# Optimization experiments

Measured on AMD Instinct MI355X. Metric: run time of the kernel, lower is better.

The kernel has to match this reference:

```python
import jax, jax.numpy as jnp
import numpy as np

N = 200_000   # total nodes across batched AIGs
E = 400_000   # edges (fan-in ~2 per gate)
D = 64        # input_dim == dim_hidden (required by in-place scatter in _gru_forward)
B = 16        # number of graphs in batch
LF = 12       # num forward topological levels
LB = 12       # num backward topological levels
NUM_ROUNDS = 1


def setup_inputs() -> dict:
    key = jax.random.key(0)
    ks = jax.random.split(key, 9)
    node_type = jax.random.randint(ks[0], (N,), 0, 3, dtype=jnp.int32)
    num_inverted_predecessors = jax.random.randint(ks[1], (N,), 0, 3, dtype=jnp.int32)
    edge_index = jax.random.randint(ks[2], (2, E), 0, N, dtype=jnp.int32)
    forward_level = jax.random.randint(ks[3], (N,), 0, LF, dtype=jnp.int32)
    backward_level = jax.random.randint(ks[4], (N,), 0, LB, dtype=jnp.int32)
    batch = jnp.sort(jax.random.randint(ks[5], (N,), 0, B, dtype=jnp.int32))
    s = 1.0 / np.sqrt(D)
    W_enc = jax.random.normal(ks[6], (2, D), dtype=jnp.float32) * 0.5
    b_enc = jnp.zeros((D,), dtype=jnp.float32)
    W_f = jax.random.normal(ks[7], (D, D), dtype=jnp.float32) * s
    b_f = jnp.zeros((D,), dtype=jnp.float32)
    W_b = jax.random.normal(ks[8], (D, D), dtype=jnp.float32) * s
    b_b = jnp.zeros((D,), dtype=jnp.float32)
    return dict(node_type=node_type,
                num_inverted_predecessors=num_inverted_predecessors,
                edge_index=edge_index,
                forward_level=forward_level,
                backward_level=backward_level,
                batch=batch,
                W_enc=W_enc, b_enc=b_enc,
                W_f=W_f, b_f=b_f,
                W_b=W_b, b_b=b_b)


def reference(node_type, num_inverted_predecessors, edge_index,
              forward_level, backward_level, batch,
              W_enc, b_enc, W_f, b_f, W_b, b_b):
    # h_init = node_encoder(cat(node_type, num_inverted_predecessors))
    x = jnp.stack([node_type, num_inverted_predecessors], axis=1).astype(W_enc.dtype)  # [N,2]
    h = x @ W_enc + b_enc  # [N,D] node_state
    src, dst = edge_index[0], edge_index[1]

    for _ in range(NUM_ROUNDS):
        # forward topological sweep: level l nodes receive sum of mlp(h_src)
        # over incoming edges whose destination is at level l (subgraph dim=1).
        for l in range(1, LF):
            m = h @ W_f + b_f                                    # AggConv mlp on current state
            e_w = (forward_level[dst] == l).astype(h.dtype)      # edges into level-l nodes
            msg = jax.ops.segment_sum(m[src] * e_w[:, None], dst, num_segments=N)
            h = jnp.where((forward_level == l)[:, None], msg, h)  # scatter l_msg into node_state
        # backward sweep (reverse flow): level-l sources receive sum of
        # mlp_b(h_dst) over outgoing edges (subgraph dim=0, target_to_source).
        for l in range(1, LB):
            m = h @ W_b + b_b
            e_w = (backward_level[src] == l).astype(h.dtype)
            msg = jax.ops.segment_sum(m[dst] * e_w[:, None], src, num_segments=N)
            h = jnp.where((backward_level == l)[:, None], msg, h)

    # readout over output nodes (node_type == 1): [global_max_pool, global_add_pool]
    out_mask = (node_type == 1)
    neg_inf = jnp.finfo(h.dtype).min
    max_pool = jax.ops.segment_max(jnp.where(out_mask[:, None], h, neg_inf), batch, num_segments=B)
    sum_pool = jax.ops.segment_sum(h * out_mask[:, None].astype(h.dtype), batch, num_segments=B)
    return jnp.concatenate([max_pool, sum_pool], axis=1)  # [B, 2*D]
```

## Files before the change

### kernel.cpp

```cpp
#include <hip/hip_runtime.h>
#include <float.h>

#define NLVL 12
#define NB   16
#define NBLK 256
#define EBLK 2048
#define FG   1024


struct Params {
    const int *nt, *ninv, *src, *dst, *fl, *bl, *batch;
    const float *We, *be, *Wf, *bf, *Wb, *bb;
    float *hN, *hB, *tabg, *out;
    int *rowptr, *cursor, *col, *nb_f, *nb_b, *onodes, *bsums, *bsums2, *meta, *plarr, *bar;
    int *deg, *rowscan;
    int *cntf, *cntb, *cnto, *blkf, *blkb, *blko;
    int *blkFf, *blkFb, *blkFo;
    int N, E, M, outN;
};

__device__ __forceinline__ float rlanef(float x, int l) {
    return __int_as_float(__builtin_amdgcn_readlane(__float_as_int(x), l));
}
__device__ __forceinline__ void sti(int* a, int v) {
    __hip_atomic_store(a, v, __ATOMIC_RELAXED, __HIP_MEMORY_SCOPE_AGENT);
}
__device__ __forceinline__ void stf(float* a, float v) {
    __hip_atomic_store(a, v, __ATOMIC_RELAXED, __HIP_MEMORY_SCOPE_AGENT);
}
__device__ __forceinline__ int ald(int* a) {
    return __hip_atomic_load(a, __ATOMIC_RELAXED, __HIP_MEMORY_SCOPE_AGENT);
}
__device__ __forceinline__ int afa(int* a, int v) {
    return __hip_atomic_fetch_add(a, v, __ATOMIC_RELAXED, __HIP_MEMORY_SCOPE_AGENT);
}

__device__ __forceinline__ void gbar3(int* bar, int nblk, int t) {
    __syncthreads();
    if (threadIdx.x == 0) {
        const int line = blockIdx.x & 15;
        const int per  = nblk >> 4;
        int a = afa(&bar[line * 32], 1);
        if (a == per * t - 1) {
            int m = afa(&bar[16 * 32], 1);
            if (m == 16 * t - 1) {
                sti(&bar[17 * 32], t);
            } else {
                while (ald(&bar[17 * 32]) < t) __builtin_amdgcn_s_sleep(1);
            }
            for (int b = line; b < nblk; b += 16)
                sti(&bar[(18 + b) * 32], t);
        } else {
            while (ald(&bar[(18 + blockIdx.x) * 32]) < t) __builtin_amdgcn_s_sleep(4);
        }
    }
    asm volatile("" ::: "memory");
    __syncthreads();
}

__device__ __forceinline__ int blockScanIncl(int v, int* s, int t) {
    s[t] = v; __syncthreads();
    for (int off = 1; off < 256; off <<= 1) {
        int add = (t >= off) ? s[t - off] : 0; __syncthreads();
        s[t] += add; __syncthreads();
    }
    int r = s[t]; __syncthreads();
    return r;
}

template <int DIR>
__device__ __forceinline__ void sweep_level(const Params& p, int lvl,
                                            const float (&w)[64], float bv,
                                            int lane, int wid, int nw, int q, int fb) {
    const int* nb = DIR ? p.nb_b : p.nb_f;
    const int* rp = p.rowptr + (DIR ? p.N : 0);
    int start = p.meta[(DIR ? 128 : 96) + lvl];
    int cnt   = p.meta[(DIR ? 128 : 96) + lvl + 1] - start;
    float* db = DIR ? p.hB : p.hN;
    const int e2 = 2 * p.E;

    int c0 = (int)((long long)cnt * wid / nw);
    int c1 = (int)((long long)cnt * (wid + 1) / nw);
    for (int i = c0; i < c1; i += 4) {
        int my = i + q;
        int v = 0, rpv = 0, rpe = 0;
        if (my < c1) {
            int e = nb[start + my];
            v = e & 0x3FFFF;
            rpv = rp[v]; rpe = rp[v + 1];
            rpv = (rpv < 0) ? 0 : (rpv > e2 ? e2 : rpv);
            rpe = (rpe < rpv) ? rpv : (rpe > e2 ? e2 : rpe);
            if (rpe > rpv + 4096) rpe = rpv + 4096;
        }
        float4 acc = make_float4(0.f, 0.f, 0.f, 0.f);
        for (int cb = rpv; cb < rpe; cb++) {
            int cu = p.col[cb];
            int u = cu & 0x3FFFF;
            int flu = (cu >> 18) & 15, blu = (cu >> 22) & 15;
            const float* sp;
            if (DIR == 0)
                sp = (flu > 0 && flu < lvl) ? (p.hN + (size_t)u * 64)
                                            : (p.tabg + ((cu >> 26) & 15) * 64);
            else
                sp = (blu > 0 && blu < lvl) ? (p.hB + (size_t)u * 64)
                   : (flu > 0)              ? (p.hN + (size_t)u * 64)
                                            : (p.tabg + ((cu >> 26) & 15) * 64);
            const float4 x = *(const float4*)(sp + fb);
            acc.x += x.x; acc.y += x.y; acc.z += x.z; acc.w += x.w;
        }
        #pragma unroll
        for (int qq = 0; qq < 4; qq++) {
            if (i + qq >= c1) break;
            int vs   = __builtin_amdgcn_readlane(v, 16 * qq);
            int degs = __builtin_amdgcn_readlane(rpe, 16 * qq)
                     - __builtin_amdgcn_readlane(rpv, 16 * qq);
            float o = bv * (float)degs;
            #pragma unroll
            for (int m = 0; m < 16; m++) {
                float ax = rlanef(acc.x, 16 * qq + m);
                float ay = rlanef(acc.y, 16 * qq + m);
                float az = rlanef(acc.z, 16 * qq + m);
                float aw = rlanef(acc.w, 16 * qq + m);
                o = fmaf(ax, w[4 * m + 0], o);
                o = fmaf(ay, w[4 * m + 1], o);
                o = fmaf(az, w[4 * m + 2], o);
                o = fmaf(aw, w[4 * m + 3], o);
            }
            stf(&db[(size_t)vs * 64 + lane], o);
        }
    }
}

__device__ inline void atomicMaxF(float* addr, float val) {
    int* ai = (int*)addr;
    int old = *ai;
    while (__int_as_float(old) < val) {
        int assumed = old;
        old = atomicCAS(ai, assumed, __float_as_int(val));
        if (old == assumed) break;
    }
}

__device__ __forceinline__ void readout_body(const Params& p, int bid, int tid) {
    int lane = tid & 63;
    int b = bid >> 5;
    int sl = bid & 31;
    int a0 = p.meta[160 + b], a1 = p.meta[161 + b];
    a0 = (a0 < 0) ? 0 : (a0 > p.N ? p.N : a0);
    a1 = (a1 < a0) ? a0 : (a1 > p.N ? p.N : a1);
    int cnt = a1 - a0;
    if (cnt == 0) return;
    int lo = a0 + (int)((long long)cnt * sl / 32);
    int hi = a0 + (int)((long long)cnt * (sl + 1) / 32);
    int wcnt = hi - lo;
    int wave = tid >> 6;
    int wl = lo + (wcnt * wave) / 4;
    int wh = lo + (wcnt * (wave + 1)) / 4;
    if (wh <= wl) return;
    float mx = -FLT_MAX, sm = 0.f;
    for (int k = wl; k < wh; k += 64) {
        int take = wh - k; if (take > 64) take = 64;
        int el = (lane < take) ? p.onodes[k + lane] : 0;
        for (int j = 0; j < take; j++) {
            int e = __shfl(el, j, 64);
            int v = e & 0x3FFFF;
            int flv = (e >> 18) & 15, blv = (e >> 22) & 15;
            const float* sp = (blv > 0) ? (p.hB + (size_t)v * 64)
                            : (flv > 0) ? (p.hN + (size_t)v * 64)
                                        : (p.tabg + ((e >> 26) & 15) * 64);
            float x = sp[lane];
            mx = fmaxf(mx, x);
            sm += x;
        }
    }
    atomicMaxF(&p.out[b * 128 + lane], mx);
    atomicAdd(&p.out[b * 128 + 64 + lane], sm);
}

__global__ __launch_bounds__(256) __attribute__((amdgpu_waves_per_eu(4, 4)))
void k_fused(Params p) {
    const int tid = threadIdx.x, bid = blockIdx.x;
    const int lane = tid & 63;
    int* bar = p.bar;
    int ep = 0;
    __shared__ int s[256];
    __shared__ int hist[40];
    __shared__ int cur[48];

    if (tid < 40) hist[tid] = 0;
    __syncthreads();
    for (int e = bid * 256 + tid; e < p.E; e += FG * 256) {
        atomicAdd(&p.deg[p.dst[e]], 1);
        atomicAdd(&p.deg[p.N + p.src[e]], 1);
    }
    for (int i = bid * 256 + tid; i < p.outN; i += FG * 256)
        stf(&p.out[i], ((i & 127) < 64) ? -FLT_MAX : 0.0f);
    if (bid == 0 && tid < 64) {
        #pragma unroll
        for (int row = 0; row < 9; row++) {
            float nf = (float)(row / 3), iv = (float)(row % 3);
            stf(&p.tabg[row * 64 + tid],
                fmaf(nf, p.We[tid], fmaf(iv, p.We[64 + tid], p.be[tid])));
        }
    }
    if (bid < NBLK) {
        int chunk = (p.N + NBLK - 1) / NBLK;
        int lo = bid * chunk, hi = lo + chunk; if (hi > p.N) hi = p.N;
        for (int i = lo + tid; i < hi; i += 256) {
            int f = p.fl[i], b = p.bl[i];
            int t2 = p.nt[i], iv = p.ninv[i];
            sti(&p.plarr[i], f | (b << 4) | ((t2 * 3 + iv) << 8));
            atomicAdd(&hist[f], 1);
            atomicAdd(&hist[12 + b], 1);
            if (t2 == 1) atomicAdd(&hist[24 + p.batch[i]], 1);
        }
    }
    __syncthreads();
    if (bid < NBLK) {
        if (tid < NLVL) { sti(&p.cntf[tid * NBLK + bid], hist[tid]); sti(&p.cntb[tid * NBLK + bid], hist[12 + tid]); }
        if (tid < NB) sti(&p.cnto[tid * NBLK + bid], hist[24 + tid]);
    }
    gbar3(bar, FG, ++ep);

    const int nscan = (p.M + 511) >> 9;
    if (bid < nscan) {
        int g0 = (bid << 9) + tid * 2;
        int e0 = (g0 < p.M) ? p.deg[g0] : 0;
        int e1 = (g0 + 1 < p.M) ? p.deg[g0 + 1] : 0;
        int incl = blockScanIncl(e0 + e1, s, tid);
        int excl = incl - (e0 + e1);
        if (g0 < p.M) sti(&p.rowscan[g0], excl);
        if (g0 + 1 < p.M) sti(&p.rowscan[g0 + 1], excl + e0);
        if (tid == 255) sti(&p.bsums[bid], incl);
    } else if (bid >= nscan + 2 && bid < nscan + 2 + 2 * NLVL + NB) {
        int j = bid - (nscan + 2);
        const int* sA; int* dA;
        if (j < NLVL)          { sA = p.cntf + j * NBLK;              dA = p.blkf + j * NBLK; }
        else if (j < 2 * NLVL) { sA = p.cntb + (j - NLVL) * NBLK;     dA = p.blkb + (j - NLVL) * NBLK; }
        else                   { sA = p.cnto + (j - 2 * NLVL) * NBLK; dA = p.blko + (j - 2 * NLVL) * NBLK; }
        int v = sA[tid];
        int incl = blockScanIncl(v, s, tid);
        sti(&dA[tid], incl - v);
        if (tid == 255) sti(&p.meta[224 + j], incl);
    }
    gbar3(bar, FG, ++ep);

    if (bid == 0) {
        int i0 = tid * 4;
        int a0 = (i0     < nscan) ? p.bsums[i0]     : 0;
        int a1 = (i0 + 1 < nscan) ? p.bsums[i0 + 1] : 0;
        int a2 = (i0 + 2 < nscan) ? p.bsums[i0 + 2] : 0;
        int a3 = (i0 + 3 < nscan) ? p.bsums[i0 + 3] : 0;
        int incl = blockScanIncl(a0 + a1 + a2 + a3, s, tid);
        int b0 = incl - (a0 + a1 + a2 + a3);
        if (i0     < nscan) sti(&p.bsums2[i0],     b0);
        if (i0 + 1 < nscan) sti(&p.bsums2[i0 + 1], b0 + a0);
        if (i0 + 2 < nscan) sti(&p.bsums2[i0 + 2], b0 + a0 + a1);
        if (i0 + 3 < nscan) sti(&p.bsums2[i0 + 3], b0 + a0 + a1 + a2);
    } else if (bid == 1 && tid < 3) {
        if (tid == 0) { int a = 0; for (int l = 0; l < NLVL; l++) { sti(&p.meta[96 + l], a);  a += p.meta[224 + l]; }            sti(&p.meta[96 + NLVL], a); }
        if (tid == 1) { int a = 0; for (int l = 0; l < NLVL; l++) { sti(&p.meta[128 + l], a); a += p.meta[224 + NLVL + l]; }     sti(&p.meta[128 + NLVL], a); }
        if (tid == 2) { int a = 0; for (int l = 0; l < NB; l++)   { sti(&p.meta[160 + l], a); a += p.meta[224 + 2 * NLVL + l]; } sti(&p.meta[160 + NB], a); }
    }
    gbar3(bar, FG, ++ep);

    for (int g = bid * 256 + tid; g < p.M; g += FG * 256) {
        int r = p.rowscan[g] + p.bsums2[g >> 9];
        sti(&p.rowptr[g], r);
        sti(&p.cursor[g], r);
    }
    if (bid == 0 && tid == 0) sti(&p.rowptr[p.M], 2 * p.E);
    for (int i = bid * 256 + tid; i < NLVL * NBLK; i += FG * 256) {
        sti(&p.blkFf[i], p.blkf[i] + p.meta[96 + (i >> 8)]);
        sti(&p.blkFb[i], p.blkb[i] + p.meta[128 + (i >> 8)]);
    }
    for (int i = bid * 256 + tid; i < NB * NBLK; i += FG * 256)
        sti(&p.blkFo[i], p.blko[i] + p.meta[160 + (i >> 8)]);
    gbar3(bar, FG, ++ep);

    for (int e = bid * 256 + tid; e < p.E; e += FG * 256) {
        int sN = p.src[e], d = p.dst[e];
        sti(&p.col[atomicAdd(&p.cursor[d], 1)],         sN | (p.plarr[sN] << 18));
        sti(&p.col[atomicAdd(&p.cursor[p.N + sN], 1)],   d | (p.plarr[d]  << 18));
    }
    if (bid < NBLK) {
        if (tid < NLVL) { cur[tid] = p.blkFf[tid * NBLK + bid]; cur[16 + tid] = p.blkFb[tid * NBLK + bid]; }
        if (tid < NB) cur[32 + tid] = p.blkFo[tid * NBLK + bid];
        __syncthreads();
        int chunk = (p.N + NBLK - 1) / NBLK;
        int lo = bid * chunk, hi = lo + chunk; if (hi > p.N) hi = p.N;
        for (int i = lo + tid; i < hi; i += 256) {
            int pl = p.plarr[i];
            int lf = pl & 15, lb = (pl >> 4) & 15, tx = (pl >> 8) & 15;
            int pk = i | (pl << 18);
            sti(&p.nb_f[atomicAdd(&cur[lf], 1)], pk);
            sti(&p.nb_b[atomicAdd(&cur[16 + lb], 1)], pk);
            if (tx >= 3 && tx < 6)
                sti(&p.onodes[atomicAdd(&cur[32 + p.batch[i]], 1)], pk);
        }
    }
    gbar3(bar, FG, ++ep);

    const int wid = (bid * 256 + tid) >> 6;
    const int nw  = (FG * 256) >> 6;
    const int q = lane >> 4, fb = (lane & 15) * 4;
    {
        float w[64];
        #pragma unroll
        for (int k = 0; k < 64; k++) w[k] = p.Wf[k * 64 + lane];
        float bv = p.bf[lane];
        for (int lvl = 1; lvl < NLVL; lvl++) {
            sweep_level<0>(p, lvl, w, bv, lane, wid, nw, q, fb);
            gbar3(bar, FG, ++ep);
        }
    }
    {
        float w[64];
        #pragma unroll
        for (int k = 0; k < 64; k++) w[k] = p.Wb[k * 64 + lane];
        float bv = p.bb[lane];
        for (int lvl = 1; lvl < NLVL; lvl++) {
            sweep_level<1>(p, lvl, w, bv, lane, wid, nw, q, fb);
            gbar3(bar, FG, ++ep);
        }
    }

    if (bid < NB * 32) readout_body(p, bid, tid);
}

__global__ void k_edge_deg(Params p) {
    int g = blockIdx.x * 256 + threadIdx.x, gs = gridDim.x * 256;
    for (int e = g; e < p.E; e += gs) {
        atomicAdd(&p.rowptr[p.dst[e]], 1);
        atomicAdd(&p.rowptr[p.N + p.src[e]], 1);
    }
}

__global__ void k_deg_hist(Params p) {
    __shared__ int hf[NLVL], hb[NLVL], ho[NB];
    int tid = threadIdx.x, bid = blockIdx.x;
    if (tid < NLVL) { hf[tid] = 0; hb[tid] = 0; }
    if (tid < NB) ho[tid] = 0;
    __syncthreads();
    int chunk = (p.N + gridDim.x - 1) / gridDim.x;
    int lo = bid * chunk, hi = lo + chunk; if (hi > p.N) hi = p.N;
    for (int i = lo + tid; i < hi; i += 256) {
        int f = p.fl[i], b = p.bl[i];
        int t = p.nt[i], iv = p.ninv[i];
        p.plarr[i] = f | (b << 4) | ((t * 3 + iv) << 8);
        atomicAdd(&hf[f], 1);
        atomicAdd(&hb[b], 1);
        if (t == 1) atomicAdd(&ho[p.batch[i]], 1);
    }
    __syncthreads();
    if (tid < NLVL) { p.cntf[tid * NBLK + bid] = hf[tid]; p.cntb[tid * NBLK + bid] = hb[tid]; }
    if (tid < NB) p.cnto[tid * NBLK + bid] = ho[tid];
}

__global__ void k_scan1(int* __restrict__ data, int M, int* __restrict__ bsums) {
    __shared__ int s[512];
    int t = threadIdx.x;
    int g = blockIdx.x * 512 + t;
    int v = (g < M) ? data[g] : 0;
    s[t] = v;
    __syncthreads();
    for (int off = 1; off < 512; off <<= 1) {
        int add = (t >= off) ? s[t - off] : 0;
        __syncthreads();
        s[t] += add;
        __syncthreads();
    }
    if (g < M) data[g] = s[t] - v;
    if (t == 511) bsums[blockIdx.x] = s[511];
}

__global__ void k_scan_top(int* __restrict__ bsums, int nblk, Params p,
                           float* __restrict__ out, int outN) {
    __shared__ int s[1024];
    __shared__ int tot[48];
    int t = threadIdx.x;
    int* meta = p.meta;
    for (int i = t; i < outN; i += 1024)
        out[i] = ((i & 127) < 64) ? -FLT_MAX : 0.0f;
    if (t < 576) {
        int row = t >> 6, j = t & 63;
        float nf = (float)(row / 3), iv = (float)(row % 3);
        p.tabg[t] = fmaf(nf, p.We[j], fmaf(iv, p.We[64 + j], p.be[j]));
    }
    int seg = t >> 8, b = t & 255;
    for (int r = 0; r < 3; r++) {
        int l = 4 * r + seg;
        int v = p.cntf[l * NBLK + b];
        s[t] = v; __syncthreads();
        for (int off = 1; off < NBLK; off <<= 1) {
            int add = (b >= off) ? s[t - off] : 0; __syncthreads();
            s[t] += add; __syncthreads();
        }
        p.blkf[l * NBLK + b] = s[t] - v;
        if (b == NBLK - 1) tot[l] = s[t];
        __syncthreads();
    }
    for (int r = 0; r < 3; r++) {
        int l = 4 * r + seg;
        int v = p.cntb[l * NBLK + b];
        s[t] = v; __syncthreads();
        for (int off = 1; off < NBLK; off <<= 1) {
            int add = (b >= off) ? s[t - off] : 0; __syncthreads();
            s[t] += add; __syncthreads();
        }
        p.blkb[l * NBLK + b] = s[t] - v;
        if (b == NBLK - 1) tot[16 + l] = s[t];
        __syncthreads();
    }
    for (int r = 0; r < 4; r++) {
        int l = 4 * r + seg;
        int v = p.cnto[l * NBLK + b];
        s[t] = v; __syncthreads();
        for (int off = 1; off < NBLK; off <<= 1) {
            int add = (b >= off) ? s[t - off] : 0; __syncthreads();
            s[t] += add; __syncthreads();
        }
        p.blko[l * NBLK + b] = s[t] - v;
        if (b == NBLK - 1) tot[32 + l] = s[t];
        __syncthreads();
    }
    if (t == 0) { int a = 0; for (int l = 0; l < NLVL; l++) { meta[96 + l] = a; a += tot[l]; } meta[96 + NLVL] = a; }
    if (t == 1) { int a = 0; for (int l = 0; l < NLVL; l++) { meta[128 + l] = a; a += tot[16 + l]; } meta[128 + NLVL] = a; }
    if (t == 2) { int a = 0; for (int l = 0; l < NB; l++) { meta[160 + l] = a; a += tot[32 + l]; } meta[160 + NB] = a; }
    __syncthreads();
    for (int i = t; i < NLVL * NBLK; i += 1024) p.blkf[i] += meta[96 + (i >> 8)];
    for (int i = t; i < NLVL * NBLK; i += 1024) p.blkb[i] += meta[128 + (i >> 8)];
    for (int i = t; i < NB * NBLK; i += 1024) p.blko[i] += meta[160 + (i >> 8)];
    int v = (t < nblk) ? bsums[t] : 0;
    s[t] = v;
    __syncthreads();
    for (int off = 1; off < 1024; off <<= 1) {
        int add = (t >= off) ? s[t - off] : 0;
        __syncthreads();
        s[t] += add;
        __syncthreads();
    }
    if (t < nblk) bsums[t] = s[t] - v;
}

__global__ void k_scan_add(int* __restrict__ rowptr, int* __restrict__ cursor, int M, int total,
                           const int* __restrict__ bsums) {
    int g = blockIdx.x * blockDim.x + threadIdx.x;
    if (g >= M) return;
    int r = rowptr[g] + bsums[g >> 9];
    rowptr[g] = r;
    cursor[g] = r;
    if (g == 0) rowptr[M] = total;
}

__global__ void k_edge_fill(Params p) {
    int g = blockIdx.x * 256 + threadIdx.x, gs = gridDim.x * 256;
    int N = p.N;
    for (int e = g; e < p.E; e += gs) {
        int s = p.src[e], d = p.dst[e];
        p.col[atomicAdd(&p.cursor[d], 1)] = s | (p.plarr[s] << 18);
        p.col[atomicAdd(&p.cursor[N + s], 1)] = d | (p.plarr[d] << 18);
    }
}

__global__ void k_fill(Params p) {
    __shared__ int cur[48];
    int tid = threadIdx.x, bid = blockIdx.x;
    int N = p.N;
    if (tid < NLVL) { cur[tid] = p.blkf[tid * NBLK + bid]; cur[16 + tid] = p.blkb[tid * NBLK + bid]; }
    if (tid < NB) cur[32 + tid] = p.blko[tid * NBLK + bid];
    __syncthreads();
    int chunk = (N + gridDim.x - 1) / gridDim.x;
    int lo = bid * chunk, hi = lo + chunk; if (hi > N) hi = N;
    for (int i = lo + tid; i < hi; i += 256) {
        int pl = p.plarr[i];
        int lf = pl & 15, lb = (pl >> 4) & 15, tx = (pl >> 8) & 15;
        int pk = i | (pl << 18);
        p.nb_f[atomicAdd(&cur[lf], 1)] = pk;
        p.nb_b[atomicAdd(&cur[16 + lb], 1)] = pk;
        if (tx >= 3 && tx < 6)
            p.onodes[atomicAdd(&cur[32 + p.batch[i]], 1)] = pk;
    }
}

__global__ __launch_bounds__(256) __attribute__((amdgpu_waves_per_eu(4, 4)))
void k_sweep(Params p, int lvl, int dir) {
    const int tid = threadIdx.x, lane = tid & 63;
    const float* W = dir ? p.Wb : p.Wf;
    float w[64];
    #pragma unroll
    for (int k = 0; k < 64; k++) w[k] = W[k * 64 + lane];
    float bv = (dir ? p.bb : p.bf)[lane];
    const int wid = (blockIdx.x * 256 + tid) >> 6;
    const int nw  = (gridDim.x * 256) >> 6;
    const int q = lane >> 4, fb = (lane & 15) * 4;
    if (dir == 0) sweep_level<0>(p, lvl, w, bv, lane, wid, nw, q, fb);
    else          sweep_level<1>(p, lvl, w, bv, lane, wid, nw, q, fb);
}

__global__ void k_readout(Params p) {
    readout_body(p, blockIdx.x, threadIdx.x);
}

extern "C" void kernel_launch(void* const* d_in, const int* in_sizes, int n_in,
                              void* d_out, int out_size, void* d_ws, size_t ws_size,
                              hipStream_t stream) {
    int N = in_sizes[0];
    int E = in_sizes[2] / 2;
    int M = 2 * N;

    Params p;
    p.nt    = (const int*)d_in[0];
    p.ninv  = (const int*)d_in[1];
    p.src   = (const int*)d_in[2];
    p.dst   = (const int*)d_in[2] + E;
    p.fl    = (const int*)d_in[3];
    p.bl    = (const int*)d_in[4];
    p.batch = (const int*)d_in[5];
    p.We    = (const float*)d_in[6];
    p.be    = (const float*)d_in[7];
    p.Wf    = (const float*)d_in[8];
    p.bf    = (const float*)d_in[9];
    p.Wb    = (const float*)d_in[10];
    p.bb    = (const float*)d_in[11];
    p.out   = (float*)d_out;
    p.N = N; p.E = E; p.M = M; p.outN = out_size;

    char* ws = (char*)d_ws;
    size_t off = 0;
    auto alloc = [&](size_t bytes) -> char* {
        char* q = ws + off;
        off = (off + bytes + 255) & ~(size_t)255;
        return q;
    };
    p.rowptr = (int*)  alloc((size_t)(M + 1) * sizeof(int));
    p.deg    = (int*)  alloc((size_t)M * sizeof(int));
    p.meta   = (int*)  alloc(512 * sizeof(int));
    p.bar    = (int*)  alloc((size_t)(18 + FG) * 32 * sizeof(int));
    size_t zbytes = (size_t)((char*)(p.bar + (18 + FG) * 32) - (char*)p.rowptr);
    p.hN     = (float*)alloc((size_t)N * 64 * sizeof(float));
    p.hB     = (float*)alloc((size_t)N * 64 * sizeof(float));
    p.tabg   = (float*)alloc(9 * 64 * sizeof(float));
    p.cursor = (int*)  alloc((size_t)M * sizeof(int));
    p.rowscan= (int*)  alloc((size_t)M * sizeof(int));
    p.col    = (int*)  alloc((size_t)2 * E * sizeof(int));
    p.nb_f   = (int*)  alloc((size_t)N * sizeof(int));
    p.nb_b   = (int*)  alloc((size_t)N * sizeof(int));
    p.onodes = (int*)  alloc((size_t)N * sizeof(int));
    p.plarr  = (int*)  alloc((size_t)N * sizeof(int));
    p.bsums  = (int*)  alloc(1024 * sizeof(int));
    p.bsums2 = (int*)  alloc(1024 * sizeof(int));
    p.cntf   = (int*)  alloc(NLVL * NBLK * sizeof(int));
    p.cntb   = (int*)  alloc(NLVL * NBLK * sizeof(int));
    p.cnto   = (int*)  alloc(NB * NBLK * sizeof(int));
    p.blkf   = (int*)  alloc(NLVL * NBLK * sizeof(int));
    p.blkb   = (int*)  alloc(NLVL * NBLK * sizeof(int));
    p.blko   = (int*)  alloc(NB * NBLK * sizeof(int));
    p.blkFf  = (int*)  alloc(NLVL * NBLK * sizeof(int));
    p.blkFb  = (int*)  alloc(NLVL * NBLK * sizeof(int));
    p.blkFo  = (int*)  alloc(NB * NBLK * sizeof(int));

    int nscan = (M + 511) / 512;

    static int g_fused = -2;
    if (g_fused == -2) {
        int mb = 0;
        g_fused = 0;
        if (hipOccupancyMaxActiveBlocksPerMultiprocessor(&mb, k_fused, 256, 0) == hipSuccess
                && mb > 0) {
            int dev = 0;
            hipGetDevice(&dev);
            hipDeviceProp_t props;
            if (hipGetDeviceProperties(&props, dev) == hipSuccess &&
                (long)mb * props.multiProcessorCount >= FG)
                g_fused = 1;
        }
    }

    hipMemsetAsync(p.rowptr, 0, zbytes, stream);
    if (g_fused == 1) {
        k_fused<<<FG, 256, 0, stream>>>(p);
    } else {
        k_edge_deg<<<EBLK, 256, 0, stream>>>(p);
        k_deg_hist<<<NBLK, 256, 0, stream>>>(p);
        k_scan1<<<nscan, 512, 0, stream>>>(p.rowptr, M, p.bsums);
        k_scan_top<<<1, 1024, 0, stream>>>(p.bsums, nscan, p, p.out, out_size);
        k_scan_add<<<(M + 255) / 256, 256, 0, stream>>>(p.rowptr, p.cursor, M, 2 * E, p.bsums);
        k_edge_fill<<<EBLK, 256, 0, stream>>>(p);
        k_fill<<<NBLK, 256, 0, stream>>>(p);
        for (int l = 1; l < NLVL; l++)
            k_sweep<<<1024, 256, 0, stream>>>(p, l, 0);
        for (int l = 1; l < NLVL; l++)
            k_sweep<<<1024, 256, 0, stream>>>(p, l, 1);
        k_readout<<<NB * 32, 256, 0, stream>>>(p);
    }
}
```

Baseline: 496.7 us.

## Spread node bucketing over all fused blocks and widen grid barrier fan-in

Node histogramming and level/batch bucketing now run on all 1024 blocks instead of only 256, so per-block count and offset arrays grow to FG entries and the offset scan handles four values per thread. The separate pass that materialised final block offsets (blkF*) and the arrays behind it are removed; each block adds the level base from meta when it loads its cursors. The grid barrier uses 32 arrival counters instead of 16, which reduces contention on each counter. The aim is shorter serial phases during CSR and bucket construction, at the cost of more, smaller histogram writes and more work in the offset scan.

```diff
diff --git a/kernel.cpp b/kernel.cpp
--- a/kernel.cpp
+++ b/kernel.cpp
@@ -6,6 +6,7 @@
 #define NBLK 256
 #define EBLK 2048
 #define FG   1024
+#define BARLINES 32
 
 
 struct Params {
@@ -15,7 +16,6 @@
     int *rowptr, *cursor, *col, *nb_f, *nb_b, *onodes, *bsums, *bsums2, *meta, *plarr, *bar;
     int *deg, *rowscan;
     int *cntf, *cntb, *cnto, *blkf, *blkb, *blko;
-    int *blkFf, *blkFb, *blkFo;
     int N, E, M, outN;
 };
 
@@ -35,23 +35,23 @@
     return __hip_atomic_fetch_add(a, v, __ATOMIC_RELAXED, __HIP_MEMORY_SCOPE_AGENT);
 }
 
-__device__ __forceinline__ void gbar3(int* bar, int nblk, int t) {
+__device__ __forceinline__ void gbar3(int* bar, int t) {
     __syncthreads();
     if (threadIdx.x == 0) {
-        const int line = blockIdx.x & 15;
-        const int per  = nblk >> 4;
+        const int line = blockIdx.x & (BARLINES - 1);
+        const int per  = FG / BARLINES;
         int a = afa(&bar[line * 32], 1);
         if (a == per * t - 1) {
-            int m = afa(&bar[16 * 32], 1);
-            if (m == 16 * t - 1) {
-                sti(&bar[17 * 32], t);
+            int m = afa(&bar[BARLINES * 32], 1);
+            if (m == BARLINES * t - 1) {
+                sti(&bar[(BARLINES + 1) * 32], t);
             } else {
-                while (ald(&bar[17 * 32]) < t) __builtin_amdgcn_s_sleep(1);
+                while (ald(&bar[(BARLINES + 1) * 32]) < t) __builtin_amdgcn_s_sleep(1);
             }
-            for (int b = line; b < nblk; b += 16)
-                sti(&bar[(18 + b) * 32], t);
+            for (int b = line; b < FG; b += BARLINES)
+                sti(&bar[(BARLINES + 2 + b) * 32], t);
         } else {
-            while (ald(&bar[(18 + blockIdx.x) * 32]) < t) __builtin_amdgcn_s_sleep(4);
+            while (ald(&bar[(BARLINES + 2 + blockIdx.x) * 32]) < t) __builtin_amdgcn_s_sleep(4);
         }
     }
     asm volatile("" ::: "memory");
@@ -203,8 +203,8 @@
                 fmaf(nf, p.We[tid], fmaf(iv, p.We[64 + tid], p.be[tid])));
         }
     }
-    if (bid < NBLK) {
-        int chunk = (p.N + NBLK - 1) / NBLK;
+    {
+        const int chunk = (p.N + FG - 1) / FG;
         int lo = bid * chunk, hi = lo + chunk; if (hi > p.N) hi = p.N;
         for (int i = lo + tid; i < hi; i += 256) {
             int f = p.fl[i], b = p.bl[i];
@@ -216,11 +216,9 @@
         }
     }
     __syncthreads();
-    if (bid < NBLK) {
-        if (tid < NLVL) { sti(&p.cntf[tid * NBLK + bid], hist[tid]); sti(&p.cntb[tid * NBLK + bid], hist[12 + tid]); }
-        if (tid < NB) sti(&p.cnto[tid * NBLK + bid], hist[24 + tid]);
-    }
-    gbar3(bar, FG, ++ep);
+    if (tid < NLVL) { sti(&p.cntf[tid * FG + bid], hist[tid]); sti(&p.cntb[tid * FG + bid], hist[12 + tid]); }
+    if (tid < NB) sti(&p.cnto[tid * FG + bid], hist[24 + tid]);
+    gbar3(bar, ++ep);
 
     const int nscan = (p.M + 511) >> 9;
     if (bid < nscan) {
@@ -235,15 +233,18 @@
     } else if (bid >= nscan + 2 && bid < nscan + 2 + 2 * NLVL + NB) {
         int j = bid - (nscan + 2);
         const int* sA; int* dA;
-        if (j < NLVL)          { sA = p.cntf + j * NBLK;              dA = p.blkf + j * NBLK; }
-        else if (j < 2 * NLVL) { sA = p.cntb + (j - NLVL) * NBLK;     dA = p.blkb + (j - NLVL) * NBLK; }
-        else                   { sA = p.cnto + (j - 2 * NLVL) * NBLK; dA = p.blko + (j - 2 * NLVL) * NBLK; }
-        int v = sA[tid];
-        int incl = blockScanIncl(v, s, tid);
-        sti(&dA[tid], incl - v);
+        if (j < NLVL)          { sA = p.cntf + j * FG;              dA = p.blkf + j * FG; }
+        else if (j < 2 * NLVL) { sA = p.cntb + (j - NLVL) * FG;     dA = p.blkb + (j - NLVL) * FG; }
+        else                   { sA = p.cnto + (j - 2 * NLVL) * FG; dA = p.blko + (j - 2 * NLVL) * FG; }
+        int i0 = tid * 4;
+        int v0 = sA[i0], v1 = sA[i0 + 1], v2 = sA[i0 + 2], v3 = sA[i0 + 3];
+        int incl = blockScanIncl(v0 + v1 + v2 + v3, s, tid);
+        int b0 = incl - (v0 + v1 + v2 + v3);
+        sti(&dA[i0], b0); sti(&dA[i0 + 1], b0 + v0);
+        sti(&dA[i0 + 2], b0 + v0 + v1); sti(&dA[i0 + 3], b0 + v0 + v1 + v2);
         if (tid == 255) sti(&p.meta[224 + j], incl);
     }
-    gbar3(bar, FG, ++ep);
+    gbar3(bar, ++ep);
 
     if (bid == 0) {
         int i0 = tid * 4;
@@ -262,7 +263,7 @@
         if (tid == 1) { int a = 0; for (int l = 0; l < NLVL; l++) { sti(&p.meta[128 + l], a); a += p.meta[224 + NLVL + l]; }     sti(&p.meta[128 + NLVL], a); }
         if (tid == 2) { int a = 0; for (int l = 0; l < NB; l++)   { sti(&p.meta[160 + l], a); a += p.meta[224 + 2 * NLVL + l]; } sti(&p.meta[160 + NB], a); }
     }
-    gbar3(bar, FG, ++ep);
+    gbar3(bar, ++ep);
 
     for (int g = bid * 256 + tid; g < p.M; g += FG * 256) {
         int r = p.rowscan[g] + p.bsums2[g >> 9];
@@ -270,24 +271,19 @@
         sti(&p.cursor[g], r);
     }
     if (bid == 0 && tid == 0) sti(&p.rowptr[p.M], 2 * p.E);
-    for (int i = bid * 256 + tid; i < NLVL * NBLK; i += FG * 256) {
-        sti(&p.blkFf[i], p.blkf[i] + p.meta[96 + (i >> 8)]);
-        sti(&p.blkFb[i], p.blkb[i] + p.meta[128 + (i >> 8)]);
-    }
-    for (int i = bid * 256 + tid; i < NB * NBLK; i += FG * 256)
-        sti(&p.blkFo[i], p.blko[i] + p.meta[160 + (i >> 8)]);
-    gbar3(bar, FG, ++ep);
+    gbar3(bar, ++ep);
 
     for (int e = bid * 256 + tid; e < p.E; e += FG * 256) {
         int sN = p.src[e], d = p.dst[e];
         sti(&p.col[atomicAdd(&p.cursor[d], 1)],         sN | (p.plarr[sN] << 18));
         sti(&p.col[atomicAdd(&p.cursor[p.N + sN], 1)],   d | (p.plarr[d]  << 18));
     }
-    if (bid < NBLK) {
-        if (tid < NLVL) { cur[tid] = p.blkFf[tid * NBLK + bid]; cur[16 + tid] = p.blkFb[tid * NBLK + bid]; }
-        if (tid < NB) cur[32 + tid] = p.blkFo[tid * NBLK + bid];
-        __syncthreads();
-        int chunk = (p.N + NBLK - 1) / NBLK;
+    if (tid < NLVL) { cur[tid] = p.blkf[tid * FG + bid] + p.meta[96 + tid];
+                      cur[16 + tid] = p.blkb[tid * FG + bid] + p.meta[128 + tid]; }
+    if (tid < NB) cur[32 + tid] = p.blko[tid * FG + bid] + p.meta[160 + tid];
+    __syncthreads();
+    {
+        const int chunk = (p.N + FG - 1) / FG;
         int lo = bid * chunk, hi = lo + chunk; if (hi > p.N) hi = p.N;
         for (int i = lo + tid; i < hi; i += 256) {
             int pl = p.plarr[i];
@@ -299,7 +295,7 @@
                 sti(&p.onodes[atomicAdd(&cur[32 + p.batch[i]], 1)], pk);
         }
     }
-    gbar3(bar, FG, ++ep);
+    gbar3(bar, ++ep);
 
     const int wid = (bid * 256 + tid) >> 6;
     const int nw  = (FG * 256) >> 6;
@@ -311,7 +307,7 @@
         float bv = p.bf[lane];
         for (int lvl = 1; lvl < NLVL; lvl++) {
             sweep_level<0>(p, lvl, w, bv, lane, wid, nw, q, fb);
-            gbar3(bar, FG, ++ep);
+            gbar3(bar, ++ep);
         }
     }
     {
@@ -321,7 +317,7 @@
         float bv = p.bb[lane];
         for (int lvl = 1; lvl < NLVL; lvl++) {
             sweep_level<1>(p, lvl, w, bv, lane, wid, nw, q, fb);
-            gbar3(bar, FG, ++ep);
+            gbar3(bar, ++ep);
         }
     }
 
@@ -536,8 +532,8 @@
     p.rowptr = (int*)  alloc((size_t)(M + 1) * sizeof(int));
     p.deg    = (int*)  alloc((size_t)M * sizeof(int));
     p.meta   = (int*)  alloc(512 * sizeof(int));
-    p.bar    = (int*)  alloc((size_t)(18 + FG) * 32 * sizeof(int));
-    size_t zbytes = (size_t)((char*)(p.bar + (18 + FG) * 32) - (char*)p.rowptr);
+    p.bar    = (int*)  alloc((size_t)(BARLINES + 2 + FG) * 32 * sizeof(int));
+    size_t zbytes = (size_t)((char*)(p.bar + (BARLINES + 2 + FG) * 32) - (char*)p.rowptr);
     p.hN     = (float*)alloc((size_t)N * 64 * sizeof(float));
     p.hB     = (float*)alloc((size_t)N * 64 * sizeof(float));
     p.tabg   = (float*)alloc(9 * 64 * sizeof(float));
@@ -550,15 +546,12 @@
     p.plarr  = (int*)  alloc((size_t)N * sizeof(int));
     p.bsums  = (int*)  alloc(1024 * sizeof(int));
     p.bsums2 = (int*)  alloc(1024 * sizeof(int));
-    p.cntf   = (int*)  alloc(NLVL * NBLK * sizeof(int));
-    p.cntb   = (int*)  alloc(NLVL * NBLK * sizeof(int));
-    p.cnto   = (int*)  alloc(NB * NBLK * sizeof(int));
-    p.blkf   = (int*)  alloc(NLVL * NBLK * sizeof(int));
-    p.blkb   = (int*)  alloc(NLVL * NBLK * sizeof(int));
-    p.blko   = (int*)  alloc(NB * NBLK * sizeof(int));
-    p.blkFf  = (int*)  alloc(NLVL * NBLK * sizeof(int));
-    p.blkFb  = (int*)  alloc(NLVL * NBLK * sizeof(int));
-    p.blkFo  = (int*)  alloc(NB * NBLK * sizeof(int));
+    p.cntf   = (int*)  alloc(NLVL * FG * sizeof(int));
+    p.cntb   = (int*)  alloc(NLVL * FG * sizeof(int));
+    p.cnto   = (int*)  alloc(NB * FG * sizeof(int));
+    p.blkf   = (int*)  alloc(NLVL * FG * sizeof(int));
+    p.blkb   = (int*)  alloc(NLVL * FG * sizeof(int));
+    p.blko   = (int*)  alloc(NB * FG * sizeof(int));
 
     int nscan = (M + 511) / 512;
 
```

Measured after the change: 498.1 us. Within noise of the previous version (+0.3%).
